# Kernel optimization log

Hardware: AMD Instinct MI355X
Metric: run time of the kernel (lower is better)

The kernel has to match this reference:

```python
import jax, jax.numpy as jnp
import numpy as np

B, L, D, H = 4, 2048, 1024, 16
HD = D // H  # head_dim = 64


def setup_inputs() -> dict:
    key = jax.random.key(0)
    k1, k2, k3 = jax.random.split(key, 3)
    x = jax.random.normal(k1, (B, L, D), dtype=jnp.float32)
    # causal mask: True where attention is NOT allowed (masked_fill semantics)
    mask = ~jnp.tril(jnp.ones((L, L), dtype=bool))
    Wqkv = jax.random.normal(k2, (3 * D, D), dtype=jnp.float32) * (1.0 / np.sqrt(D))
    bqkv = jnp.zeros((3 * D,), dtype=jnp.float32)
    Wo = jax.random.normal(k3, (D, D), dtype=jnp.float32) * (1.0 / np.sqrt(D))
    bo = jnp.zeros((D,), dtype=jnp.float32)
    return {"x": x, "mask": mask, "Wqkv": Wqkv, "bqkv": bqkv, "Wo": Wo, "bo": bo}


def reference(x, mask, Wqkv, bqkv, Wo, bo):
    b, l, d = x.shape
    qkv = jnp.einsum('bld,ed->ble', x, Wqkv) + bqkv            # [b, l, 3d]
    q, k, v = jnp.split(qkv, 3, axis=-1)
    q = q.reshape(b, l, H, HD).transpose(0, 2, 1, 3)           # [b, h, l, hd]
    k = k.reshape(b, l, H, HD).transpose(0, 2, 1, 3)
    v = v.reshape(b, l, H, HD).transpose(0, 2, 1, 3)
    scale = 1.0 / jnp.sqrt(jnp.float32(HD))
    a = jnp.einsum('bhqd,bhkd->bhqk', q, k) * scale            # [b, h, l, l]
    a = jnp.where(mask, -jnp.inf, a)
    a = jax.nn.softmax(a, axis=-1)
    out = jnp.einsum('bhqk,bhkd->bhqd', a, v)                  # [b, h, l, hd]
    out = out.transpose(0, 2, 1, 3).reshape(b, l, d)
    return jnp.einsum('bld,ed->ble', out, Wo) + bo
```

## Files before the change

### kernel.cpp

```cpp
#include <hip/hip_runtime.h>

typedef __attribute__((ext_vector_type(8))) short short8;
typedef __attribute__((ext_vector_type(4))) float f32x4;
typedef __attribute__((ext_vector_type(16))) float f32x16;
typedef __attribute__((ext_vector_type(2))) int int2v;
typedef __attribute__((ext_vector_type(4))) int int4v;
typedef unsigned short u16;
typedef unsigned int u32;

#define B_ 4
#define L_ 2048
#define D_ 1024
#define H_ 16
#define HD_ 64

__device__ __forceinline__ void load_lds16(const void* g, void* l) {
  __builtin_amdgcn_global_load_lds(
      (__attribute__((address_space(1))) unsigned int*)(g),
      (__attribute__((address_space(3))) unsigned int*)(l),
      16, 0, 0);
}

__device__ __forceinline__ u16 f2bf(float f) {
  union { float f; unsigned u; } c; c.f = f;
  unsigned r = c.u + 0x7FFFu + ((c.u >> 16) & 1u);
  return (u16)(r >> 16);
}

__device__ __forceinline__ u32 cvtpk(float a, float b) {
  u32 r; asm("v_cvt_pk_bf16_f32 %0, %1, %2" : "=v"(r) : "v"(a), "v"(b)); return r;
}

__device__ __forceinline__ int2v trread(u32 addr) {
  int2v r; asm volatile("ds_read_b64_tr_b16 %0, %1" : "=v"(r) : "v"(addr)); return r;
}

__global__ __launch_bounds__(256) void cvt_bf16(const float* __restrict__ in,
                                                u16* __restrict__ out, int n) {
  int i = (blockIdx.x * 256 + threadIdx.x) * 4;
  if (i >= n) return;
  float4 v = *(const float4*)(in + i);
  u16 o0 = f2bf(v.x), o1 = f2bf(v.y), o2 = f2bf(v.z), o3 = f2bf(v.w);
  u16* p = out + i;
  p[0] = o0; p[1] = o1; p[2] = o2; p[3] = o3;
}

template <bool BF16_OUT>
__global__ __launch_bounds__(256, 2) void gemm_bt(
    const u16* __restrict__ A, const u16* __restrict__ B,
    const float* __restrict__ bias, void* __restrict__ Cout,
    int M, int N, int K) {
  __shared__ u16 Asm[128 * 32];
  __shared__ u16 Bsm[128 * 32];
  const int tid = threadIdx.x;
  const int lane = tid & 63;
  const int wid = tid >> 6;
  const int fr = lane & 15, fq = lane >> 4;
  const int wr = wid >> 1, wc = wid & 1;
  const long m0 = (long)blockIdx.y * 128;
  const long n0 = (long)blockIdx.x * 128;
  const int srow = lane >> 2;
  const int scol = (lane & 3) * 8;

  f32x4 acc[4][4] = {};

  for (int kt = 0; kt < K; kt += 32) {
    __syncthreads();
#pragma unroll
    for (int c = 0; c < 2; ++c) {
      const int sec = wid * 2 + c;
      load_lds16(A + (m0 + sec * 16 + srow) * K + kt + scol,
                 (char*)Asm + sec * 1024);
      load_lds16(B + (n0 + sec * 16 + srow) * K + kt + scol,
                 (char*)Bsm + sec * 1024);
    }
    __syncthreads();
    short8 af[4], bfr[4];
#pragma unroll
    for (int m = 0; m < 4; ++m)
      af[m] = *(const short8*)((const char*)Asm + (wr * 64 + m * 16 + fr) * 64 + fq * 16);
#pragma unroll
    for (int n = 0; n < 4; ++n)
      bfr[n] = *(const short8*)((const char*)Bsm + (wc * 64 + n * 16 + fr) * 64 + fq * 16);
#pragma unroll
    for (int m = 0; m < 4; ++m)
#pragma unroll
      for (int n = 0; n < 4; ++n)
        acc[m][n] = __builtin_amdgcn_mfma_f32_16x16x32_bf16(af[m], bfr[n], acc[m][n], 0, 0, 0);
  }

  float bv[4];
#pragma unroll
  for (int n = 0; n < 4; ++n) bv[n] = bias[n0 + wc * 64 + n * 16 + fr];

#pragma unroll
  for (int m = 0; m < 4; ++m) {
#pragma unroll
    for (int n = 0; n < 4; ++n) {
      const long col = n0 + wc * 64 + n * 16 + fr;
#pragma unroll
      for (int r = 0; r < 4; ++r) {
        const long row = m0 + wr * 64 + m * 16 + fq * 4 + r;
        float v = acc[m][n][r] + bv[n];
        if (BF16_OUT)
          ((u16*)Cout)[row * N + col] = f2bf(v);
        else
          ((float*)Cout)[row * N + col] = v;
      }
    }
  }
}

__global__ __launch_bounds__(256, 2) void flash_attn3(
    const u16* __restrict__ qkv, u16* __restrict__ attn) {
  __shared__ u16 K2[2][64 * 64];
  __shared__ u16 V2[2][64 * 64];

  const int tid = threadIdx.x;
  const int lane = tid & 63;
  const int wid = tid >> 6;
  const int l31 = lane & 31;
  const int h = lane >> 5;

  const int lin = blockIdx.y * 8 + blockIdx.x;
  const int bh = (lin & 7) * 8 + ((lin >> 3) & 7);
  const int x = lin >> 6;
  const int qa = x, qb = 15 - x;
  const long rowbase = (long)(bh >> 4) * L_;
  const int hh = bh & 15;

  const int wq0A = qa * 128 + wid * 32;
  const int wq0B = qb * 128 + wid * 32;
  const int qgA = wq0A + l31;
  const int qgB = wq0B + l31;

  short8 qfA[4], qfB[4];
  {
    const u16* qpA = qkv + (rowbase + qgA) * 3072 + hh * 64 + h * 8;
    const u16* qpB = qkv + (rowbase + qgB) * 3072 + hh * 64 + h * 8;
#pragma unroll
    for (int ks = 0; ks < 4; ++ks) {
      qfA[ks] = *(const short8*)(qpA + ks * 16);
      qfB[ks] = *(const short8*)(qpB + ks * 16);
    }
  }

  int krow[2], kvv[2], dvv[2];
#pragma unroll
  for (int c = 0; c < 2; ++c) {
    const int s = (wid * 2 + c) * 8 + (lane >> 3);
    krow[c] = s;
    kvv[c] = ((s >> 2) << 2) + ((lane >> 1) & 3);
    dvv[c] = ((s & 3) << 4) + ((lane & 1) << 3);
  }
  const int kchunk = ((lane & 7) ^ (lane >> 3)) * 8;

  const u32 Vaddr = (u32)(unsigned long long)(__attribute__((address_space(3))) char*)(void*)&V2[0][0];
  const u32 vb0 = Vaddr + ((lane >> 4) & 1) * 128 + (lane & 15) * 8 + h * 1024;

  f32x16 oA[2] = {}, oB[2] = {};
  float mA = -__builtin_inff(), lA = 0.f;
  float mB = -__builtin_inff(), lB = 0.f;
  const float SC2 = 0.125f * 1.4426950408889634f;

  auto stage = [&](int kt, int buf) {
    const long ktb = (long)kt * 64;
#pragma unroll
    for (int c = 0; c < 2; ++c) {
      load_lds16(qkv + (rowbase + ktb + krow[c]) * 3072 + 1024 + hh * 64 + kchunk,
                 (char*)&K2[buf][0] + (wid * 2 + c) * 1024);
      load_lds16(qkv + (rowbase + ktb + kvv[c]) * 3072 + 2048 + hh * 64 + dvv[c],
                 (char*)&V2[buf][0] + (wid * 2 + c) * 1024);
    }
  };

  auto computeTile = [&](int ktb, int cur, const short8* qf, int wq0, int qg,
                         f32x16* o, float& m_r, float& l_r) {
    if (ktb > wq0 + 31) return;
    const char* Kb = (const char*)&K2[cur][0];
    const u32 vbB = vb0 + (u32)cur * 8192;

    f32x16 p[2];
    __builtin_amdgcn_s_setprio(1);
#pragma unroll
    for (int t = 0; t < 2; ++t) {
      f32x16 acc = {};
#pragma unroll
      for (int ks = 0; ks < 4; ++ks) {
        const int row = t * 32 + l31;
        short8 kf = *(const short8*)(Kb + row * 128 + (((ks * 2 + h) ^ (row & 7)) * 16));
        acc = __builtin_amdgcn_mfma_f32_32x32x16_bf16(kf, qf[ks], acc, 0, 0, 0);
      }
      p[t] = acc;
    }
    __builtin_amdgcn_s_setprio(0);

    if (ktb + 63 > wq0) {
#pragma unroll
      for (int t = 0; t < 2; ++t)
#pragma unroll
        for (int r = 0; r < 16; ++r) {
          const int kvg = ktb + t * 32 + (r & 3) + 8 * (r >> 2) + 4 * h;
          p[t][r] = (kvg > qg) ? -__builtin_inff() : p[t][r];
        }
    }

    float a[16];
#pragma unroll
    for (int r = 0; r < 16; ++r) a[r] = fmaxf(p[0][r], p[1][r]);
#pragma unroll
    for (int s = 8; s > 0; s >>= 1)
#pragma unroll
      for (int r = 0; r < s; ++r) a[r] = fmaxf(a[r], a[r + s]);
    const float mt = fmaxf(a[0], __shfl_xor(a[0], 32));

    const float m_new = fmaxf(m_r, mt);
    const float alpha = __builtin_exp2f((m_r - m_new) * SC2);
    const float msc = m_new * SC2;
#pragma unroll
    for (int t = 0; t < 2; ++t)
#pragma unroll
      for (int r = 0; r < 16; ++r)
        p[t][r] = __builtin_exp2f(fmaf(p[t][r], SC2, -msc));

    float b2[16];
#pragma unroll
    for (int r = 0; r < 16; ++r) b2[r] = p[0][r] + p[1][r];
#pragma unroll
    for (int s = 8; s > 0; s >>= 1)
#pragma unroll
      for (int r = 0; r < s; ++r) b2[r] += b2[r + s];
    const float rs = b2[0] + __shfl_xor(b2[0], 32);

    l_r = alpha * l_r + rs;
    m_r = m_new;
#pragma unroll
    for (int t = 0; t < 2; ++t)
#pragma unroll
      for (int r = 0; r < 16; ++r) o[t][r] *= alpha;

    u32 pf[4][4];
#pragma unroll
    for (int t = 0; t < 2; ++t)
#pragma unroll
      for (int ksl = 0; ksl < 2; ++ksl) {
        const u32 x0 = cvtpk(p[t][8 * ksl + 0], p[t][8 * ksl + 1]);
        const u32 x1 = cvtpk(p[t][8 * ksl + 2], p[t][8 * ksl + 3]);
        const u32 y0 = cvtpk(p[t][8 * ksl + 4], p[t][8 * ksl + 5]);
        const u32 y1 = cvtpk(p[t][8 * ksl + 6], p[t][8 * ksl + 7]);
        const u32 r0 = (u32)__shfl_xor((int)(h ? x0 : y0), 32);
        const u32 r1 = (u32)__shfl_xor((int)(h ? x1 : y1), 32);
        const int ks = t * 2 + ksl;
        pf[ks][0] = h ? r0 : x0;
        pf[ks][1] = h ? r1 : x1;
        pf[ks][2] = h ? y0 : r0;
        pf[ks][3] = h ? y1 : r1;
      }

#pragma unroll
    for (int dt = 0; dt < 2; ++dt) {
      int2v vf[8];
#pragma unroll
      for (int ks = 0; ks < 4; ++ks) {
        vf[ks * 2 + 0] = trread(vbB + dt * 256 + ks * 2048);
        vf[ks * 2 + 1] = trread(vbB + dt * 256 + ks * 2048 + 512);
      }
      asm volatile("s_waitcnt lgkmcnt(0)" ::: "memory");
      __builtin_amdgcn_sched_barrier(0);
      __builtin_amdgcn_s_setprio(1);
#pragma unroll
      for (int ks = 0; ks < 4; ++ks) {
        int4v av;
        av[0] = vf[ks * 2][0]; av[1] = vf[ks * 2][1];
        av[2] = vf[ks * 2 + 1][0]; av[3] = vf[ks * 2 + 1][1];
        int4v pv;
        pv[0] = (int)pf[ks][0]; pv[1] = (int)pf[ks][1];
        pv[2] = (int)pf[ks][2]; pv[3] = (int)pf[ks][3];
        o[dt] = __builtin_amdgcn_mfma_f32_32x32x16_bf16(
            __builtin_bit_cast(short8, av), __builtin_bit_cast(short8, pv),
            o[dt], 0, 0, 0);
      }
      __builtin_amdgcn_s_setprio(0);
    }
  };

  stage(0, 0);
  __syncthreads();
  int cur = 0;
  const int kmB = 2 * qb + 1, kmA = 2 * qa + 1;
  for (int kt = 0; kt <= kmB; ++kt) {
    if (kt < kmB) stage(kt + 1, cur ^ 1);
    computeTile(kt * 64, cur, qfB, wq0B, qgB, oB, mB, lB);
    if (kt <= kmA) computeTile(kt * 64, cur, qfA, wq0A, qgA, oA, mA, lA);
    __syncthreads();
    cur ^= 1;
  }

  {
    const float invl = 1.0f / lB;
    u16* orow = attn + (rowbase + qgB) * 1024 + hh * 64;
#pragma unroll
    for (int t = 0; t < 2; ++t)
#pragma unroll
      for (int rp = 0; rp < 8; ++rp) {
        const int r0 = rp * 2;
        const u32 w = cvtpk(oB[t][r0] * invl, oB[t][r0 + 1] * invl);
        const int d = t * 32 + (r0 & 3) + 8 * (r0 >> 2) + 4 * h;
        *(u32*)(orow + d) = w;
      }
  }
  {
    const float invl = 1.0f / lA;
    u16* orow = attn + (rowbase + qgA) * 1024 + hh * 64;
#pragma unroll
    for (int t = 0; t < 2; ++t)
#pragma unroll
      for (int rp = 0; rp < 8; ++rp) {
        const int r0 = rp * 2;
        const u32 w = cvtpk(oA[t][r0] * invl, oA[t][r0 + 1] * invl);
        const int d = t * 32 + (r0 & 3) + 8 * (r0 >> 2) + 4 * h;
        *(u32*)(orow + d) = w;
      }
  }
}

extern "C" void kernel_launch(void* const* d_in, const int* in_sizes, int n_in,
                              void* d_out, int out_size, void* d_ws, size_t ws_size,
                              hipStream_t stream) {
  const float* x    = (const float*)d_in[0];
  const float* Wqkv = (const float*)d_in[2];
  const float* bqkv = (const float*)d_in[3];
  const float* Wo   = (const float*)d_in[4];
  const float* bo   = (const float*)d_in[5];
  float* out = (float*)d_out;

  const long ML = (long)B_ * L_;
  u16* xb    = (u16*)d_ws;
  u16* wqkvb = xb + ML * D_;
  u16* wob   = wqkvb + (long)3 * D_ * D_;
  u16* qkv   = wob + (long)D_ * D_;
  u16* attn  = qkv + ML * 3 * D_;

  cvt_bf16<<<dim3((int)(ML * D_ / 1024)), 256, 0, stream>>>(x, xb, (int)(ML * D_));
  cvt_bf16<<<dim3(3 * D_ * D_ / 1024), 256, 0, stream>>>(Wqkv, wqkvb, 3 * D_ * D_);
  cvt_bf16<<<dim3(D_ * D_ / 1024), 256, 0, stream>>>(Wo, wob, D_ * D_);

  gemm_bt<true><<<dim3(3 * D_ / 128, (int)(ML / 128)), 256, 0, stream>>>(
      xb, wqkvb, bqkv, qkv, (int)ML, 3 * D_, D_);

  flash_attn3<<<dim3(8, B_ * H_), 256, 0, stream>>>(qkv, attn);

  gemm_bt<false><<<dim3(D_ / 128, (int)(ML / 128)), 256, 0, stream>>>(
      attn, wob, bo, out, (int)ML, D_, D_);
}
```

Baseline: 192.5 us.

## Double attention KV tile to 128 keys, add lazy rescale and permlane swap

The flash attention kernel now stages 128-key K/V tiles instead of 64, which halves the number of loop iterations and barriers and doubles MFMA work per tile. The online softmax skips the rescale of the output accumulator and row sum unless the new max exceeds the old one by a threshold, in the style of FA4 lazy rescaling. The cross-half P exchange uses v_permlane32_swap instead of shuffles. In exchange, LDS use and register pressure roughly double, and more fully masked work is done because the per-warp causal early exit was removed and the diagonal tiles are coarser.

Measured after the change: 196.9 us. +2.3%, slower.

```diff
diff --git a/kernel.cpp b/kernel.cpp
--- a/kernel.cpp
+++ b/kernel.cpp
@@ -33,6 +33,16 @@
 
 __device__ __forceinline__ int2v trread(u32 addr) {
   int2v r; asm volatile("ds_read_b64_tr_b16 %0, %1" : "=v"(r) : "v"(addr)); return r;
+}
+
+__device__ __forceinline__ void pswap(u32& a, u32& b) {
+  asm("v_permlane32_swap_b32 %0, %1" : "+v"(a), "+v"(b));
+}
+__device__ __forceinline__ float xhalf_max(float x) {
+  return fmaxf(x, __shfl_xor(x, 32));
+}
+__device__ __forceinline__ float xhalf_sum(float x) {
+  return x + __shfl_xor(x, 32);
 }
 
 __global__ __launch_bounds__(256) void cvt_bf16(const float* __restrict__ in,
@@ -111,10 +121,10 @@
   }
 }
 
-__global__ __launch_bounds__(256, 2) void flash_attn3(
+__global__ __launch_bounds__(256, 2) void flash_attn5(
     const u16* __restrict__ qkv, u16* __restrict__ attn) {
-  __shared__ u16 K2[2][64 * 64];
-  __shared__ u16 V2[2][64 * 64];
+  __shared__ u16 K2[2][128 * 64];
+  __shared__ u16 V2[2][128 * 64];
 
   const int tid = threadIdx.x;
   const int lane = tid & 63;
@@ -145,10 +155,10 @@
     }
   }
 
-  int krow[2], kvv[2], dvv[2];
-#pragma unroll
-  for (int c = 0; c < 2; ++c) {
-    const int s = (wid * 2 + c) * 8 + (lane >> 3);
+  int krow[4], kvv[4], dvv[4];
+#pragma unroll
+  for (int c = 0; c < 4; ++c) {
+    const int s = (wid * 4 + c) * 8 + (lane >> 3);
     krow[c] = s;
     kvv[c] = ((s >> 2) << 2) + ((lane >> 1) & 3);
     dvv[c] = ((s & 3) << 4) + ((lane & 1) << 3);
@@ -164,26 +174,25 @@
   const float SC2 = 0.125f * 1.4426950408889634f;
 
   auto stage = [&](int kt, int buf) {
-    const long ktb = (long)kt * 64;
-#pragma unroll
-    for (int c = 0; c < 2; ++c) {
+    const long ktb = (long)kt * 128;
+#pragma unroll
+    for (int c = 0; c < 4; ++c) {
       load_lds16(qkv + (rowbase + ktb + krow[c]) * 3072 + 1024 + hh * 64 + kchunk,
-                 (char*)&K2[buf][0] + (wid * 2 + c) * 1024);
+                 (char*)&K2[buf][0] + (wid * 4 + c) * 1024);
       load_lds16(qkv + (rowbase + ktb + kvv[c]) * 3072 + 2048 + hh * 64 + dvv[c],
-                 (char*)&V2[buf][0] + (wid * 2 + c) * 1024);
+                 (char*)&V2[buf][0] + (wid * 4 + c) * 1024);
     }
   };
 
   auto computeTile = [&](int ktb, int cur, const short8* qf, int wq0, int qg,
                          f32x16* o, float& m_r, float& l_r) {
-    if (ktb > wq0 + 31) return;
     const char* Kb = (const char*)&K2[cur][0];
-    const u32 vbB = vb0 + (u32)cur * 8192;
-
-    f32x16 p[2];
+    const u32 vbB = vb0 + (u32)cur * 16384;
+
+    f32x16 p[4];
     __builtin_amdgcn_s_setprio(1);
 #pragma unroll
-    for (int t = 0; t < 2; ++t) {
+    for (int t = 0; t < 4; ++t) {
       f32x16 acc = {};
 #pragma unroll
       for (int ks = 0; ks < 4; ++ks) {
@@ -195,9 +204,9 @@
     }
     __builtin_amdgcn_s_setprio(0);
 
-    if (ktb + 63 > wq0) {
-#pragma unroll
-      for (int t = 0; t < 2; ++t)
+    if (ktb + 127 > wq0) {
+#pragma unroll
+      for (int t = 0; t < 4; ++t)
 #pragma unroll
         for (int r = 0; r < 16; ++r) {
           const int kvg = ktb + t * 32 + (r & 3) + 8 * (r >> 2) + 4 * h;
@@ -207,61 +216,61 @@
 
     float a[16];
 #pragma unroll
-    for (int r = 0; r < 16; ++r) a[r] = fmaxf(p[0][r], p[1][r]);
+    for (int r = 0; r < 16; ++r)
+      a[r] = fmaxf(fmaxf(p[0][r], p[1][r]), fmaxf(p[2][r], p[3][r]));
 #pragma unroll
     for (int s = 8; s > 0; s >>= 1)
 #pragma unroll
       for (int r = 0; r < s; ++r) a[r] = fmaxf(a[r], a[r + s]);
-    const float mt = fmaxf(a[0], __shfl_xor(a[0], 32));
-
-    const float m_new = fmaxf(m_r, mt);
-    const float alpha = __builtin_exp2f((m_r - m_new) * SC2);
-    const float msc = m_new * SC2;
-#pragma unroll
-    for (int t = 0; t < 2; ++t)
+    const float mt = xhalf_max(a[0]);
+
+    if (!__all(mt - m_r <= 44.0f)) {
+      const float m_new = fmaxf(m_r, mt);
+      const float alpha = __builtin_exp2f((m_r - m_new) * SC2);
+#pragma unroll
+      for (int t = 0; t < 2; ++t)
+#pragma unroll
+        for (int r = 0; r < 16; ++r) o[t][r] *= alpha;
+      l_r *= alpha;
+      m_r = m_new;
+    }
+    const float msc = m_r * SC2;
+#pragma unroll
+    for (int t = 0; t < 4; ++t)
 #pragma unroll
       for (int r = 0; r < 16; ++r)
         p[t][r] = __builtin_exp2f(fmaf(p[t][r], SC2, -msc));
 
     float b2[16];
 #pragma unroll
-    for (int r = 0; r < 16; ++r) b2[r] = p[0][r] + p[1][r];
+    for (int r = 0; r < 16; ++r)
+      b2[r] = (p[0][r] + p[1][r]) + (p[2][r] + p[3][r]);
 #pragma unroll
     for (int s = 8; s > 0; s >>= 1)
 #pragma unroll
       for (int r = 0; r < s; ++r) b2[r] += b2[r + s];
-    const float rs = b2[0] + __shfl_xor(b2[0], 32);
-
-    l_r = alpha * l_r + rs;
-    m_r = m_new;
-#pragma unroll
-    for (int t = 0; t < 2; ++t)
-#pragma unroll
-      for (int r = 0; r < 16; ++r) o[t][r] *= alpha;
-
-    u32 pf[4][4];
-#pragma unroll
-    for (int t = 0; t < 2; ++t)
+    l_r += xhalf_sum(b2[0]);
+
+    u32 pf[8][4];
+#pragma unroll
+    for (int t = 0; t < 4; ++t)
 #pragma unroll
       for (int ksl = 0; ksl < 2; ++ksl) {
-        const u32 x0 = cvtpk(p[t][8 * ksl + 0], p[t][8 * ksl + 1]);
-        const u32 x1 = cvtpk(p[t][8 * ksl + 2], p[t][8 * ksl + 3]);
-        const u32 y0 = cvtpk(p[t][8 * ksl + 4], p[t][8 * ksl + 5]);
-        const u32 y1 = cvtpk(p[t][8 * ksl + 6], p[t][8 * ksl + 7]);
-        const u32 r0 = (u32)__shfl_xor((int)(h ? x0 : y0), 32);
-        const u32 r1 = (u32)__shfl_xor((int)(h ? x1 : y1), 32);
+        u32 x0 = cvtpk(p[t][8 * ksl + 0], p[t][8 * ksl + 1]);
+        u32 x1 = cvtpk(p[t][8 * ksl + 2], p[t][8 * ksl + 3]);
+        u32 y0 = cvtpk(p[t][8 * ksl + 4], p[t][8 * ksl + 5]);
+        u32 y1 = cvtpk(p[t][8 * ksl + 6], p[t][8 * ksl + 7]);
+        pswap(x0, y0);
+        pswap(x1, y1);
         const int ks = t * 2 + ksl;
-        pf[ks][0] = h ? r0 : x0;
-        pf[ks][1] = h ? r1 : x1;
-        pf[ks][2] = h ? y0 : r0;
-        pf[ks][3] = h ? y1 : r1;
+        pf[ks][0] = x0; pf[ks][1] = x1; pf[ks][2] = y0; pf[ks][3] = y1;
       }
 
 #pragma unroll
     for (int dt = 0; dt < 2; ++dt) {
-      int2v vf[8];
-#pragma unroll
-      for (int ks = 0; ks < 4; ++ks) {
+      int2v vf[16];
+#pragma unroll
+      for (int ks = 0; ks < 8; ++ks) {
         vf[ks * 2 + 0] = trread(vbB + dt * 256 + ks * 2048);
         vf[ks * 2 + 1] = trread(vbB + dt * 256 + ks * 2048 + 512);
       }
@@ -269,7 +278,7 @@
       __builtin_amdgcn_sched_barrier(0);
       __builtin_amdgcn_s_setprio(1);
 #pragma unroll
-      for (int ks = 0; ks < 4; ++ks) {
+      for (int ks = 0; ks < 8; ++ks) {
         int4v av;
         av[0] = vf[ks * 2][0]; av[1] = vf[ks * 2][1];
         av[2] = vf[ks * 2 + 1][0]; av[3] = vf[ks * 2 + 1][1];
@@ -287,11 +296,10 @@
   stage(0, 0);
   __syncthreads();
   int cur = 0;
-  const int kmB = 2 * qb + 1, kmA = 2 * qa + 1;
-  for (int kt = 0; kt <= kmB; ++kt) {
-    if (kt < kmB) stage(kt + 1, cur ^ 1);
-    computeTile(kt * 64, cur, qfB, wq0B, qgB, oB, mB, lB);
-    if (kt <= kmA) computeTile(kt * 64, cur, qfA, wq0A, qgA, oA, mA, lA);
+  for (int kt = 0; kt <= qb; ++kt) {
+    if (kt < qb) stage(kt + 1, cur ^ 1);
+    computeTile(kt * 128, cur, qfB, wq0B, qgB, oB, mB, lB);
+    if (kt <= qa) computeTile(kt * 128, cur, qfA, wq0A, qgA, oA, mA, lA);
     __syncthreads();
     cur ^= 1;
   }
@@ -348,7 +356,7 @@
   gemm_bt<true><<<dim3(3 * D_ / 128, (int)(ML / 128)), 256, 0, stream>>>(
       xb, wqkvb, bqkv, qkv, (int)ML, 3 * D_, D_);
 
-  flash_attn3<<<dim3(8, B_ * H_), 256, 0, stream>>>(qkv, attn);
+  flash_attn5<<<dim3(8, B_ * H_), 256, 0, stream>>>(qkv, attn);
 
   gemm_bt<false><<<dim3(D_ / 128, (int)(ML / 128)), 256, 0, stream>>>(
       attn, wob, bo, out, (int)ML, D_, D_);
```

## Restructure flash attention work split, add lazy rescale and permlane swap

Applied to the files above, without the earlier changes.

The attention kernel is reorganized so each block pairs two 64-row query tiles (one early, one late) with one tile per wave pair, instead of each wave carrying two query sets. The grid grows from 512 to 1024 blocks, and launch bounds rise to allow 4 blocks per CU, which halves per-thread accumulator state and raises occupancy. The online softmax now skips the rescale of the output accumulator when the running max grows by less than a threshold. The cross-half shuffle is replaced by v_permlane32_swap. Risks are that waves in a block get uneven work, with early-tile waves idling at barriers, and that K/V is reloaded more times overall.

After: 200.5 us. 1.04x slower.

```diff
diff --git a/kernel.cpp b/kernel.cpp
--- a/kernel.cpp
+++ b/kernel.cpp
@@ -33,6 +33,16 @@
 
 __device__ __forceinline__ int2v trread(u32 addr) {
   int2v r; asm volatile("ds_read_b64_tr_b16 %0, %1" : "=v"(r) : "v"(addr)); return r;
+}
+
+__device__ __forceinline__ void pswap(u32& a, u32& b) {
+  asm("v_permlane32_swap_b32 %0, %1" : "+v"(a), "+v"(b));
+}
+__device__ __forceinline__ float xhalf_max(float x) {
+  return fmaxf(x, __shfl_xor(x, 32));
+}
+__device__ __forceinline__ float xhalf_sum(float x) {
+  return x + __shfl_xor(x, 32);
 }
 
 __global__ __launch_bounds__(256) void cvt_bf16(const float* __restrict__ in,
@@ -111,7 +121,7 @@
   }
 }
 
-__global__ __launch_bounds__(256, 2) void flash_attn3(
+__global__ __launch_bounds__(256, 4) void flash_attn6(
     const u16* __restrict__ qkv, u16* __restrict__ attn) {
   __shared__ u16 K2[2][64 * 64];
   __shared__ u16 V2[2][64 * 64];
@@ -122,27 +132,20 @@
   const int l31 = lane & 31;
   const int h = lane >> 5;
 
-  const int lin = blockIdx.y * 8 + blockIdx.x;
-  const int bh = (lin & 7) * 8 + ((lin >> 3) & 7);
-  const int x = lin >> 6;
-  const int qa = x, qb = 15 - x;
+  const int bh = blockIdx.x;
+  const int x = blockIdx.y;
   const long rowbase = (long)(bh >> 4) * L_;
   const int hh = bh & 15;
 
-  const int wq0A = qa * 128 + wid * 32;
-  const int wq0B = qb * 128 + wid * 32;
-  const int qgA = wq0A + l31;
-  const int qgB = wq0B + l31;
-
-  short8 qfA[4], qfB[4];
+  const int tbase = (wid < 2) ? (31 - x) * 64 : x * 64;
+  const int wq0 = tbase + (wid & 1) * 32;
+  const int qg = wq0 + l31;
+
+  short8 qf[4];
   {
-    const u16* qpA = qkv + (rowbase + qgA) * 3072 + hh * 64 + h * 8;
-    const u16* qpB = qkv + (rowbase + qgB) * 3072 + hh * 64 + h * 8;
-#pragma unroll
-    for (int ks = 0; ks < 4; ++ks) {
-      qfA[ks] = *(const short8*)(qpA + ks * 16);
-      qfB[ks] = *(const short8*)(qpB + ks * 16);
-    }
+    const u16* qp = qkv + (rowbase + qg) * 3072 + hh * 64 + h * 8;
+#pragma unroll
+    for (int ks = 0; ks < 4; ++ks) qf[ks] = *(const short8*)(qp + ks * 16);
   }
 
   int krow[2], kvv[2], dvv[2];
@@ -158,9 +161,8 @@
   const u32 Vaddr = (u32)(unsigned long long)(__attribute__((address_space(3))) char*)(void*)&V2[0][0];
   const u32 vb0 = Vaddr + ((lane >> 4) & 1) * 128 + (lane & 15) * 8 + h * 1024;
 
-  f32x16 oA[2] = {}, oB[2] = {};
-  float mA = -__builtin_inff(), lA = 0.f;
-  float mB = -__builtin_inff(), lB = 0.f;
+  f32x16 o[2] = {};
+  float m_r = -__builtin_inff(), l_r = 0.f;
   const float SC2 = 0.125f * 1.4426950408889634f;
 
   auto stage = [&](int kt, int buf) {
@@ -174,154 +176,133 @@
     }
   };
 
-  auto computeTile = [&](int ktb, int cur, const short8* qf, int wq0, int qg,
-                         f32x16* o, float& m_r, float& l_r) {
-    if (ktb > wq0 + 31) return;
-    const char* Kb = (const char*)&K2[cur][0];
-    const u32 vbB = vb0 + (u32)cur * 8192;
-
-    f32x16 p[2];
-    __builtin_amdgcn_s_setprio(1);
-#pragma unroll
-    for (int t = 0; t < 2; ++t) {
-      f32x16 acc = {};
-#pragma unroll
-      for (int ks = 0; ks < 4; ++ks) {
-        const int row = t * 32 + l31;
-        short8 kf = *(const short8*)(Kb + row * 128 + (((ks * 2 + h) ^ (row & 7)) * 16));
-        acc = __builtin_amdgcn_mfma_f32_32x32x16_bf16(kf, qf[ks], acc, 0, 0, 0);
-      }
-      p[t] = acc;
-    }
-    __builtin_amdgcn_s_setprio(0);
-
-    if (ktb + 63 > wq0) {
-#pragma unroll
-      for (int t = 0; t < 2; ++t)
-#pragma unroll
-        for (int r = 0; r < 16; ++r) {
-          const int kvg = ktb + t * 32 + (r & 3) + 8 * (r >> 2) + 4 * h;
-          p[t][r] = (kvg > qg) ? -__builtin_inff() : p[t][r];
-        }
-    }
-
-    float a[16];
-#pragma unroll
-    for (int r = 0; r < 16; ++r) a[r] = fmaxf(p[0][r], p[1][r]);
-#pragma unroll
-    for (int s = 8; s > 0; s >>= 1)
-#pragma unroll
-      for (int r = 0; r < s; ++r) a[r] = fmaxf(a[r], a[r + s]);
-    const float mt = fmaxf(a[0], __shfl_xor(a[0], 32));
-
-    const float m_new = fmaxf(m_r, mt);
-    const float alpha = __builtin_exp2f((m_r - m_new) * SC2);
-    const float msc = m_new * SC2;
-#pragma unroll
-    for (int t = 0; t < 2; ++t)
-#pragma unroll
-      for (int r = 0; r < 16; ++r)
-        p[t][r] = __builtin_exp2f(fmaf(p[t][r], SC2, -msc));
-
-    float b2[16];
-#pragma unroll
-    for (int r = 0; r < 16; ++r) b2[r] = p[0][r] + p[1][r];
-#pragma unroll
-    for (int s = 8; s > 0; s >>= 1)
-#pragma unroll
-      for (int r = 0; r < s; ++r) b2[r] += b2[r + s];
-    const float rs = b2[0] + __shfl_xor(b2[0], 32);
-
-    l_r = alpha * l_r + rs;
-    m_r = m_new;
-#pragma unroll
-    for (int t = 0; t < 2; ++t)
-#pragma unroll
-      for (int r = 0; r < 16; ++r) o[t][r] *= alpha;
-
-    u32 pf[4][4];
-#pragma unroll
-    for (int t = 0; t < 2; ++t)
-#pragma unroll
-      for (int ksl = 0; ksl < 2; ++ksl) {
-        const u32 x0 = cvtpk(p[t][8 * ksl + 0], p[t][8 * ksl + 1]);
-        const u32 x1 = cvtpk(p[t][8 * ksl + 2], p[t][8 * ksl + 3]);
-        const u32 y0 = cvtpk(p[t][8 * ksl + 4], p[t][8 * ksl + 5]);
-        const u32 y1 = cvtpk(p[t][8 * ksl + 6], p[t][8 * ksl + 7]);
-        const u32 r0 = (u32)__shfl_xor((int)(h ? x0 : y0), 32);
-        const u32 r1 = (u32)__shfl_xor((int)(h ? x1 : y1), 32);
-        const int ks = t * 2 + ksl;
-        pf[ks][0] = h ? r0 : x0;
-        pf[ks][1] = h ? r1 : x1;
-        pf[ks][2] = h ? y0 : r0;
-        pf[ks][3] = h ? y1 : r1;
-      }
-
-#pragma unroll
-    for (int dt = 0; dt < 2; ++dt) {
-      int2v vf[8];
-#pragma unroll
-      for (int ks = 0; ks < 4; ++ks) {
-        vf[ks * 2 + 0] = trread(vbB + dt * 256 + ks * 2048);
-        vf[ks * 2 + 1] = trread(vbB + dt * 256 + ks * 2048 + 512);
-      }
-      asm volatile("s_waitcnt lgkmcnt(0)" ::: "memory");
-      __builtin_amdgcn_sched_barrier(0);
-      __builtin_amdgcn_s_setprio(1);
-#pragma unroll
-      for (int ks = 0; ks < 4; ++ks) {
-        int4v av;
-        av[0] = vf[ks * 2][0]; av[1] = vf[ks * 2][1];
-        av[2] = vf[ks * 2 + 1][0]; av[3] = vf[ks * 2 + 1][1];
-        int4v pv;
-        pv[0] = (int)pf[ks][0]; pv[1] = (int)pf[ks][1];
-        pv[2] = (int)pf[ks][2]; pv[3] = (int)pf[ks][3];
-        o[dt] = __builtin_amdgcn_mfma_f32_32x32x16_bf16(
-            __builtin_bit_cast(short8, av), __builtin_bit_cast(short8, pv),
-            o[dt], 0, 0, 0);
-      }
-      __builtin_amdgcn_s_setprio(0);
-    }
-  };
-
+  const int ktm = 31 - x;
   stage(0, 0);
   __syncthreads();
   int cur = 0;
-  const int kmB = 2 * qb + 1, kmA = 2 * qa + 1;
-  for (int kt = 0; kt <= kmB; ++kt) {
-    if (kt < kmB) stage(kt + 1, cur ^ 1);
-    computeTile(kt * 64, cur, qfB, wq0B, qgB, oB, mB, lB);
-    if (kt <= kmA) computeTile(kt * 64, cur, qfA, wq0A, qgA, oA, mA, lA);
+  for (int kt = 0; kt <= ktm; ++kt) {
+    if (kt < ktm) stage(kt + 1, cur ^ 1);
+    const int ktb = kt * 64;
+    if (ktb <= wq0 + 31) {
+      const char* Kb = (const char*)&K2[cur][0];
+      const u32 vbB = vb0 + (u32)cur * 8192;
+
+      f32x16 p[2];
+      __builtin_amdgcn_s_setprio(1);
+#pragma unroll
+      for (int t = 0; t < 2; ++t) {
+        f32x16 acc = {};
+#pragma unroll
+        for (int ks = 0; ks < 4; ++ks) {
+          const int row = t * 32 + l31;
+          short8 kf = *(const short8*)(Kb + row * 128 + (((ks * 2 + h) ^ (row & 7)) * 16));
+          acc = __builtin_amdgcn_mfma_f32_32x32x16_bf16(kf, qf[ks], acc, 0, 0, 0);
+        }
+        p[t] = acc;
+      }
+      __builtin_amdgcn_s_setprio(0);
+
+      if (ktb + 63 > wq0) {
+#pragma unroll
+        for (int t = 0; t < 2; ++t)
+#pragma unroll
+          for (int r = 0; r < 16; ++r) {
+            const int kvg = ktb + t * 32 + (r & 3) + 8 * (r >> 2) + 4 * h;
+            p[t][r] = (kvg > qg) ? -__builtin_inff() : p[t][r];
+          }
+      }
+
+      float a[16];
+#pragma unroll
+      for (int r = 0; r < 16; ++r) a[r] = fmaxf(p[0][r], p[1][r]);
+#pragma unroll
+      for (int s = 8; s > 0; s >>= 1)
+#pragma unroll
+        for (int r = 0; r < s; ++r) a[r] = fmaxf(a[r], a[r + s]);
+      const float mt = xhalf_max(a[0]);
+
+      if (!__all(mt - m_r <= 44.0f)) {
+        const float m_new = fmaxf(m_r, mt);
+        const float alpha = __builtin_exp2f((m_r - m_new) * SC2);
+#pragma unroll
+        for (int t = 0; t < 2; ++t)
+#pragma unroll
+          for (int r = 0; r < 16; ++r) o[t][r] *= alpha;
+        l_r *= alpha;
+        m_r = m_new;
+      }
+      const float msc = m_r * SC2;
+#pragma unroll
+      for (int t = 0; t < 2; ++t)
+#pragma unroll
+        for (int r = 0; r < 16; ++r)
+          p[t][r] = __builtin_exp2f(fmaf(p[t][r], SC2, -msc));
+
+      float b2[16];
+#pragma unroll
+      for (int r = 0; r < 16; ++r) b2[r] = p[0][r] + p[1][r];
+#pragma unroll
+      for (int s = 8; s > 0; s >>= 1)
+#pragma unroll
+        for (int r = 0; r < s; ++r) b2[r] += b2[r + s];
+      l_r += xhalf_sum(b2[0]);
+
+      u32 pf[4][4];
+#pragma unroll
+      for (int t = 0; t < 2; ++t)
+#pragma unroll
+        for (int ksl = 0; ksl < 2; ++ksl) {
+          u32 x0 = cvtpk(p[t][8 * ksl + 0], p[t][8 * ksl + 1]);
+          u32 x1 = cvtpk(p[t][8 * ksl + 2], p[t][8 * ksl + 3]);
+          u32 y0 = cvtpk(p[t][8 * ksl + 4], p[t][8 * ksl + 5]);
+          u32 y1 = cvtpk(p[t][8 * ksl + 6], p[t][8 * ksl + 7]);
+          pswap(x0, y0);
+          pswap(x1, y1);
+          const int ks = t * 2 + ksl;
+          pf[ks][0] = x0; pf[ks][1] = x1; pf[ks][2] = y0; pf[ks][3] = y1;
+        }
+
+#pragma unroll
+      for (int dt = 0; dt < 2; ++dt) {
+        int2v vf[8];
+#pragma unroll
+        for (int ks = 0; ks < 4; ++ks) {
+          vf[ks * 2 + 0] = trread(vbB + dt * 256 + ks * 2048);
+          vf[ks * 2 + 1] = trread(vbB + dt * 256 + ks * 2048 + 512);
+        }
+        asm volatile("s_waitcnt lgkmcnt(0)" ::: "memory");
+        __builtin_amdgcn_sched_barrier(0);
+        __builtin_amdgcn_s_setprio(1);
+#pragma unroll
+        for (int ks = 0; ks < 4; ++ks) {
+          int4v av;
+          av[0] = vf[ks * 2][0]; av[1] = vf[ks * 2][1];
+          av[2] = vf[ks * 2 + 1][0]; av[3] = vf[ks * 2 + 1][1];
+          int4v pv;
+          pv[0] = (int)pf[ks][0]; pv[1] = (int)pf[ks][1];
+          pv[2] = (int)pf[ks][2]; pv[3] = (int)pf[ks][3];
+          o[dt] = __builtin_amdgcn_mfma_f32_32x32x16_bf16(
+              __builtin_bit_cast(short8, av), __builtin_bit_cast(short8, pv),
+              o[dt], 0, 0, 0);
+        }
+        __builtin_amdgcn_s_setprio(0);
+      }
+    }
     __syncthreads();
     cur ^= 1;
   }
 
-  {
-    const float invl = 1.0f / lB;
-    u16* orow = attn + (rowbase + qgB) * 1024 + hh * 64;
-#pragma unroll
-    for (int t = 0; t < 2; ++t)
-#pragma unroll
-      for (int rp = 0; rp < 8; ++rp) {
-        const int r0 = rp * 2;
-        const u32 w = cvtpk(oB[t][r0] * invl, oB[t][r0 + 1] * invl);
-        const int d = t * 32 + (r0 & 3) + 8 * (r0 >> 2) + 4 * h;
-        *(u32*)(orow + d) = w;
-      }
-  }
-  {
-    const float invl = 1.0f / lA;
-    u16* orow = attn + (rowbase + qgA) * 1024 + hh * 64;
-#pragma unroll
-    for (int t = 0; t < 2; ++t)
-#pragma unroll
-      for (int rp = 0; rp < 8; ++rp) {
-        const int r0 = rp * 2;
-        const u32 w = cvtpk(oA[t][r0] * invl, oA[t][r0 + 1] * invl);
-        const int d = t * 32 + (r0 & 3) + 8 * (r0 >> 2) + 4 * h;
-        *(u32*)(orow + d) = w;
-      }
-  }
+  const float invl = 1.0f / l_r;
+  u16* orow = attn + (rowbase + qg) * 1024 + hh * 64;
+#pragma unroll
+  for (int t = 0; t < 2; ++t)
+#pragma unroll
+    for (int rp = 0; rp < 8; ++rp) {
+      const int r0 = rp * 2;
+      const u32 w = cvtpk(o[t][r0] * invl, o[t][r0 + 1] * invl);
+      const int d = t * 32 + (r0 & 3) + 8 * (r0 >> 2) + 4 * h;
+      *(u32*)(orow + d) = w;
+    }
 }
 
 extern "C" void kernel_launch(void* const* d_in, const int* in_sizes, int n_in,
@@ -348,7 +329,7 @@
   gemm_bt<true><<<dim3(3 * D_ / 128, (int)(ML / 128)), 256, 0, stream>>>(
       xb, wqkvb, bqkv, qkv, (int)ML, 3 * D_, D_);
 
-  flash_attn3<<<dim3(8, B_ * H_), 256, 0, stream>>>(qkv, attn);
+  flash_attn6<<<dim3(64, 16), 256, 0, stream>>>(qkv, attn);
 
   gemm_bt<false><<<dim3(D_ / 128, (int)(ML / 128)), 256, 0, stream>>>(
       attn, wob, bo, out, (int)ML, D_, D_);
```
